# Optimization experiments

Measured on AMD Instinct MI355X. Metric: run time of the kernel, lower is better.

The kernel has to match this reference:

```python
import jax, jax.numpy as jnp
import numpy as np

TEMP = 0.07
POS_WINDOW = 2
EPS = 1e-8
NEG = -1e9  # finite large-negative for masking (safe under vjp)


def _l2norm(x):
    # matches F.normalize(dim=-1) with eps=1e-12
    n = jnp.sqrt(jnp.sum(x * x, axis=-1, keepdims=True))
    return x / jnp.maximum(n, 1e-12)


def setup_inputs() -> dict:
    key = jax.random.key(0)
    k1, k2, k3, k4, k5 = jax.random.split(key, 5)
    B, T, D = 32, 1024, 256
    eeg_enc = jax.random.normal(k1, (B, T, D), dtype=jnp.float32)
    eye_enc = jax.random.normal(k2, (B, T, D), dtype=jnp.float32)
    mask = jax.random.randint(k3, (B, T), 0, 2, dtype=jnp.int32)
    W_eeg = jax.random.normal(k4, (D, D), dtype=jnp.float32) / np.sqrt(D)
    W_eye = jax.random.normal(k5, (D, D), dtype=jnp.float32) / np.sqrt(D)
    return {"eeg_enc": eeg_enc, "eye_enc": eye_enc, "mask": mask,
            "W_eeg": W_eeg, "W_eye": W_eye}


def reference(eeg_enc, eye_enc, mask, W_eeg, W_eye):
    B, T, D = eeg_enc.shape
    valid = mask > 0  # (B,T)
    # nn.Linear(bias=False): x @ W.T, then L2-normalize
    e = _l2norm(jnp.einsum('btd,ed->bte', eeg_enc, W_eeg))
    v = _l2norm(jnp.einsum('btd,ed->bte', eye_enc, W_eye))
    sims = jnp.einsum('bid,bjd->bij', e, v) / TEMP  # (B,T,T)
    # rank of each valid step within the compressed (gathered) ordering
    rank = jnp.cumsum(valid.astype(jnp.int32), axis=-1) - 1  # (B,T)
    band = jnp.abs(rank[:, :, None] - rank[:, None, :]) <= POS_WINDOW
    pair = valid[:, :, None] & valid[:, None, :]  # both steps valid
    pos = pair & band
    # per-row max over positive (banded) entries
    pos_scores = jnp.max(jnp.where(pos, sims, NEG), axis=-1)  # (B,T)
    # logsumexp over valid columns (the gathered sims row)
    lse = jax.nn.logsumexp(jnp.where(valid[:, None, :], sims, NEG), axis=-1)
    row_loss = -(pos_scores - lse)  # (B,T)
    Tv = jnp.sum(valid, axis=-1)  # (B,)
    per_b = jnp.sum(jnp.where(valid, row_loss, 0.0), axis=-1) / jnp.maximum(Tv, 1)
    per_b = jnp.where(Tv >= 2, per_b, 0.0)  # skip samples with <2 valid steps
    return jnp.sum(per_b) / (B + EPS)
```

## Files before the change

### kernel.cpp

```cpp
#include <hip/hip_runtime.h>
#include <hip/hip_bf16.h>

typedef __attribute__((ext_vector_type(8))) short bf16x8;
typedef __attribute__((ext_vector_type(4))) float f32x4;

#define INVT (1.0f/0.07f)

static __device__ __forceinline__ short f2bf(float f){
    unsigned int u = __float_as_uint(f);
    unsigned int r = (u + 0x7fffu + ((u >> 16) & 1u)) >> 16;
    return (short)r;
}
static __device__ __forceinline__ float bf2f(short s){
    return __uint_as_float(((unsigned int)(unsigned short)s) << 16);
}

__global__ __launch_bounds__(256) void wconv_kernel(const float* __restrict__ Weeg,
                                                    const float* __restrict__ Weye,
                                                    short* __restrict__ Wout){
    int i = blockIdx.x * 256 + threadIdx.x;
    float v = (i < 65536) ? Weeg[i] : Weye[i - 65536];
    Wout[i] = f2bf(v);
}

__global__ __launch_bounds__(256) void rank_kernel(const int* __restrict__ mask,
                                                   int* __restrict__ rank,
                                                   int* __restrict__ idx,
                                                   int* __restrict__ Tv,
                                                   float* __restrict__ cb){
    __shared__ int ssum[256];
    int b = blockIdx.x, tid = threadIdx.x;
    int local[4]; int s = 0;
    #pragma unroll
    for (int q = 0; q < 4; ++q){
        int t = tid*4 + q;
        local[q] = (mask[b*1024 + t] > 0) ? 1 : 0;
        s += local[q];
    }
    ssum[tid] = s;
    __syncthreads();
    for (int off = 1; off < 256; off <<= 1){
        int add = (tid >= off) ? ssum[tid - off] : 0;
        __syncthreads();
        ssum[tid] += add;
        __syncthreads();
    }
    int run = ssum[tid] - s;
    #pragma unroll
    for (int q = 0; q < 4; ++q){
        int t = tid*4 + q;
        int g = b*1024 + t;
        run += local[q];
        rank[g] = run - 1;
        cb[g]   = local[q] ? 0.0f : -1e9f;
        if (local[q]) idx[b*1024 + run - 1] = t;
    }
    if (tid == 255) Tv[b] = ssum[255];
}

__global__ __launch_bounds__(256, 3) void proj_kernel(const float* __restrict__ Aeeg,
                                                      const float* __restrict__ Aeye,
                                                      const short* __restrict__ Wbf,
                                                      short* __restrict__ Eout,
                                                      short* __restrict__ Vout){
    __shared__ short sW[64 * 264];
    int sel = blockIdx.y;
    const float* A   = sel ? Aeye : Aeeg;
    const short* W   = Wbf + sel * 65536;
    short*       Out = sel ? Vout : Eout;

    int tid = threadIdx.x;
    int w = tid >> 6, lane = tid & 63;
    int l15 = lane & 15, lq = lane >> 4;
    int kb  = lq * 8;
    int row0 = blockIdx.x * 64;

    bf16x8 af[8];
    {
        const float* ap = A + (size_t)(row0 + w*16 + l15) * 256 + kb;
        #pragma unroll
        for (int g = 0; g < 8; ++g){
            float4 x0 = *(const float4*)(ap + g*32);
            float4 x1 = *(const float4*)(ap + g*32 + 4);
            bf16x8 t;
            t[0]=f2bf(x0.x); t[1]=f2bf(x0.y); t[2]=f2bf(x0.z); t[3]=f2bf(x0.w);
            t[4]=f2bf(x1.x); t[5]=f2bf(x1.y); t[6]=f2bf(x1.z); t[7]=f2bf(x1.w);
            af[g] = t;
        }
    }

    f32x4 acc[16];
    #pragma unroll
    for (int q = 0; q < 16; ++q) acc[q] = (f32x4){0.f,0.f,0.f,0.f};

    for (int pass = 0; pass < 4; ++pass){
        if (pass) __syncthreads();
        #pragma unroll
        for (int p = 0; p < 8; ++p){
            int flat = p*2048 + tid*8;
            int r = flat >> 8, c = flat & 255;
            *(int4*)&sW[r*264 + c] = *(const int4*)(W + (size_t)(pass*64 + r)*256 + c);
        }
        __syncthreads();
        #pragma unroll
        for (int nt = 0; nt < 4; ++nt){
            f32x4 c = acc[pass*4 + nt];
            const short* wp = &sW[(nt*16 + l15) * 264 + kb];
            #pragma unroll
            for (int g = 0; g < 8; ++g){
                bf16x8 bf = *(const bf16x8*)(wp + g*32);
                c = __builtin_amdgcn_mfma_f32_16x16x32_bf16(af[g], bf, c, 0, 0, 0);
            }
            acc[pass*4 + nt] = c;
        }
    }

    float scale[4];
    #pragma unroll
    for (int r = 0; r < 4; ++r){
        float ss = 0.f;
        #pragma unroll
        for (int q = 0; q < 16; ++q){ float x = acc[q][r]; ss += x*x; }
        ss += __shfl_xor(ss, 1);
        ss += __shfl_xor(ss, 2);
        ss += __shfl_xor(ss, 4);
        ss += __shfl_xor(ss, 8);
        scale[r] = 1.0f / fmaxf(sqrtf(ss), 1e-12f);
    }

    short* op = Out + (size_t)(row0 + w*16) * 256;
    #pragma unroll
    for (int q = 0; q < 16; ++q){
        #pragma unroll
        for (int r = 0; r < 4; ++r){
            op[(lq*4 + r) * 256 + q*16 + l15] = f2bf(acc[q][r] * scale[r]);
        }
    }
}

__global__ __launch_bounds__(256, 3) void loss_kernel(const short* __restrict__ E,
                                                      const short* __restrict__ V,
                                                      const float* __restrict__ cb,
                                                      float* __restrict__ psum){
    __shared__ short sV[64 * 264];
    __shared__ float sCb[256];

    int ib = blockIdx.x;
    int js = blockIdx.y;
    int b  = blockIdx.z;
    int i0 = ib * 128;

    int tid = threadIdx.x;
    int w = tid >> 6, lane = tid & 63;
    int l15 = lane & 15, lq = lane >> 4;
    int kb = lq * 8;

    sCb[tid] = cb[b*1024 + js*256 + tid];

    bf16x8 af0[8], af1[8];
    {
        const short* ep = E + ((size_t)b*1024 + i0 + w*32 + l15) * 256 + kb;
        #pragma unroll
        for (int g = 0; g < 8; ++g){
            af0[g] = *(const bf16x8*)(ep + g*32);
            af1[g] = *(const bf16x8*)(ep + 16*256 + g*32);
        }
    }

    float ls0[4] = {0.f,0.f,0.f,0.f};
    float ls1[4] = {0.f,0.f,0.f,0.f};
    const short* vb = V + ((size_t)b*1024 + js*256) * 256;

    for (int jc = 0; jc < 4; ++jc){
        __syncthreads();
        #pragma unroll
        for (int p = 0; p < 8; ++p){
            int flat = p*2048 + tid*8;
            int r = flat >> 8, c = flat & 255;
            *(int4*)&sV[r*264 + c] = *(const int4*)(vb + (size_t)(jc*64 + r)*256 + c);
        }
        __syncthreads();

        #pragma unroll
        for (int jt = 0; jt < 4; ++jt){
            f32x4 c0 = {0.f,0.f,0.f,0.f};
            f32x4 c1 = {0.f,0.f,0.f,0.f};
            const short* vp = &sV[(jt*16 + l15) * 264 + kb];
            #pragma unroll
            for (int g = 0; g < 8; ++g){
                bf16x8 bf = *(const bf16x8*)(vp + g*32);
                c0 = __builtin_amdgcn_mfma_f32_16x16x32_bf16(af0[g], bf, c0, 0, 0, 0);
                c1 = __builtin_amdgcn_mfma_f32_16x16x32_bf16(af1[g], bf, c1, 0, 0, 0);
            }
            float cbj = sCb[jc*64 + jt*16 + l15];
            #pragma unroll
            for (int r = 0; r < 4; ++r){
                ls0[r] += __expf(fmaf(c0[r], INVT, cbj));
                ls1[r] += __expf(fmaf(c1[r], INVT, cbj));
            }
        }
    }

    #pragma unroll
    for (int r = 0; r < 4; ++r){
        #pragma unroll
        for (int m = 1; m < 16; m <<= 1){
            ls0[r] += __shfl_xor(ls0[r], m);
            ls1[r] += __shfl_xor(ls1[r], m);
        }
    }
    if (l15 == 0){
        float* pp = psum + (((size_t)(b*4 + js)) << 10);
        int ibase = i0 + w*32 + lq*4;
        #pragma unroll
        for (int r = 0; r < 4; ++r){
            pp[ibase + r]      = ls0[r];
            pp[ibase + 16 + r] = ls1[r];
        }
    }
}

__global__ __launch_bounds__(256) void pos_kernel(const short* __restrict__ E,
                                                  const short* __restrict__ V,
                                                  const int* __restrict__ mask,
                                                  const int* __restrict__ rank,
                                                  const int* __restrict__ idx,
                                                  const int* __restrict__ Tv,
                                                  float* __restrict__ pmax){
    int tid = threadIdx.x;
    int gl  = tid & 15;
    int gid = (blockIdx.x * 256 + tid) >> 4;

    for (int q = 0; q < 8; ++q){
        int rf = gid + q * 4096;
        int b  = rf >> 10;
        if (mask[rf] > 0){
            int ri = rank[rf];
            int tv = Tv[b];
            int lo = ri - 2; if (lo < 0) lo = 0;
            int hi = ri + 2; if (hi > tv - 1) hi = tv - 1;

            const short* epp = E + (size_t)rf * 256 + gl * 16;
            float ev[16];
            {
                bf16x8 e0 = *(const bf16x8*)epp;
                bf16x8 e1 = *(const bf16x8*)(epp + 8);
                #pragma unroll
                for (int k = 0; k < 8; ++k){ ev[k] = bf2f(e0[k]); ev[8+k] = bf2f(e1[k]); }
            }
            float pm = -1e30f;
            for (int r = lo; r <= hi; ++r){
                int j = idx[b*1024 + r];
                const short* vpp = V + ((size_t)(b*1024) + j) * 256 + gl * 16;
                bf16x8 v0 = *(const bf16x8*)vpp;
                bf16x8 v1 = *(const bf16x8*)(vpp + 8);
                float s = 0.f;
                #pragma unroll
                for (int k = 0; k < 8; ++k){
                    s = fmaf(ev[k],   bf2f(v0[k]), s);
                    s = fmaf(ev[8+k], bf2f(v1[k]), s);
                }
                s += __shfl_xor(s, 1);
                s += __shfl_xor(s, 2);
                s += __shfl_xor(s, 4);
                s += __shfl_xor(s, 8);
                pm = fmaxf(pm, s);
            }
            if (gl == 0) pmax[rf] = pm * INVT;
        }
    }
}

__global__ __launch_bounds__(256) void reduce_kernel(const float* __restrict__ psum,
                                                     const float* __restrict__ pmax,
                                                     const int* __restrict__ mask,
                                                     const int* __restrict__ Tv,
                                                     float* __restrict__ per_b){
    __shared__ float sred[4];
    int b = blockIdx.x, tid = threadIdx.x;
    float a = 0.f;
    const float* pp = psum + (((size_t)(b*4)) << 10);
    #pragma unroll
    for (int q = 0; q < 4; ++q){
        int i = q*256 + tid;
        int g = b*1024 + i;
        if (mask[g] > 0){
            float ps = pp[i] + pp[i + 1024] + pp[i + 2048] + pp[i + 3072];
            a += logf(ps) - pmax[g];
        }
    }
    #pragma unroll
    for (int m = 1; m < 64; m <<= 1) a += __shfl_xor(a, m);
    if ((tid & 63) == 0) sred[tid >> 6] = a;
    __syncthreads();
    if (tid == 0){
        float t = sred[0] + sred[1] + sred[2] + sred[3];
        int tv = Tv[b];
        per_b[b] = (tv >= 2) ? t / (float)tv : 0.f;
    }
}

__global__ void final_kernel(const float* __restrict__ per_b,
                             float* __restrict__ out){
    int tid = threadIdx.x;
    float v = (tid < 32) ? per_b[tid] : 0.f;
    #pragma unroll
    for (int m = 1; m < 64; m <<= 1) v += __shfl_xor(v, m);
    if (tid == 0) out[0] = v / 32.0f;
}

extern "C" void kernel_launch(void* const* d_in, const int* in_sizes, int n_in,
                              void* d_out, int out_size, void* d_ws, size_t ws_size,
                              hipStream_t stream) {
    const float* eeg  = (const float*)d_in[0];
    const float* eye  = (const float*)d_in[1];
    const int*   mask = (const int*)d_in[2];
    const float* Weeg = (const float*)d_in[3];
    const float* Weye = (const float*)d_in[4];
    float* out = (float*)d_out;

    char* ws = (char*)d_ws;
    short* e_bf  = (short*)(ws);
    short* v_bf  = (short*)(ws + 16777216);
    short* wbf   = (short*)(ws + 33554432);
    int*   rank  = (int*)  (ws + 33816576);
    int*   idx   = (int*)  (ws + 33947648);
    float* cb    = (float*)(ws + 34078720);
    float* psum  = (float*)(ws + 34209792);
    float* pmax  = (float*)(ws + 34734080);
    int*   Tv    = (int*)  (ws + 34865152);
    float* per_b = (float*)(ws + 34865280);

    wconv_kernel<<<512, 256, 0, stream>>>(Weeg, Weye, wbf);
    rank_kernel<<<32, 256, 0, stream>>>(mask, rank, idx, Tv, cb);
    proj_kernel<<<dim3(512, 2), 256, 0, stream>>>(eeg, eye, wbf, e_bf, v_bf);
    loss_kernel<<<dim3(8, 4, 32), 256, 0, stream>>>(e_bf, v_bf, cb, psum);
    pos_kernel<<<256, 256, 0, stream>>>(e_bf, v_bf, mask, rank, idx, Tv, pmax);
    reduce_kernel<<<32, 256, 0, stream>>>(psum, pmax, mask, Tv, per_b);
    final_kernel<<<1, 64, 0, stream>>>(per_b, out);
}
```

Measured before the change: 186.6 us.

## Fuse prep kernels, transpose proj MFMA for vector stores, enlarge loss tile, flatten pos grid

Merges the weight-conversion and rank kernels into one launch to cut launch overhead. The projection now swaps the MFMA operands so each lane holds a row's outputs, which allows packed short4 stores and a two-step row-norm shuffle. The loss kernel processes 256 query rows per block instead of 128, reusing each shared V tile across four MFMA streams, with occupancy lowered to 2 blocks per SM to fit the extra registers. The positive-score kernel drops its inner loop and launches one 16-lane group per row across more blocks. The risk is register pressure in the loss kernel and fewer blocks in that grid.

```diff
diff --git a/kernel.cpp b/kernel.cpp
--- a/kernel.cpp
+++ b/kernel.cpp
@@ -15,21 +15,23 @@
     return __uint_as_float(((unsigned int)(unsigned short)s) << 16);
 }
 
-__global__ __launch_bounds__(256) void wconv_kernel(const float* __restrict__ Weeg,
-                                                    const float* __restrict__ Weye,
-                                                    short* __restrict__ Wout){
-    int i = blockIdx.x * 256 + threadIdx.x;
-    float v = (i < 65536) ? Weeg[i] : Weye[i - 65536];
-    Wout[i] = f2bf(v);
-}
-
-__global__ __launch_bounds__(256) void rank_kernel(const int* __restrict__ mask,
+__global__ __launch_bounds__(256) void prep_kernel(const float* __restrict__ Weeg,
+                                                   const float* __restrict__ Weye,
+                                                   const int* __restrict__ mask,
+                                                   short* __restrict__ Wout,
                                                    int* __restrict__ rank,
                                                    int* __restrict__ idx,
                                                    int* __restrict__ Tv,
                                                    float* __restrict__ cb){
     __shared__ int ssum[256];
-    int b = blockIdx.x, tid = threadIdx.x;
+    int tid = threadIdx.x;
+    if (blockIdx.x < 512){
+        int i = blockIdx.x * 256 + tid;
+        float v = (i < 65536) ? Weeg[i] : Weye[i - 65536];
+        Wout[i] = f2bf(v);
+        return;
+    }
+    int b = blockIdx.x - 512;
     int local[4]; int s = 0;
     #pragma unroll
     for (int q = 0; q < 4; ++q){
@@ -75,7 +77,7 @@
     int kb  = lq * 8;
     int row0 = blockIdx.x * 64;
 
-    bf16x8 af[8];
+    bf16x8 xf[8];
     {
         const float* ap = A + (size_t)(row0 + w*16 + l15) * 256 + kb;
         #pragma unroll
@@ -85,7 +87,7 @@
             bf16x8 t;
             t[0]=f2bf(x0.x); t[1]=f2bf(x0.y); t[2]=f2bf(x0.z); t[3]=f2bf(x0.w);
             t[4]=f2bf(x1.x); t[5]=f2bf(x1.y); t[6]=f2bf(x1.z); t[7]=f2bf(x1.w);
-            af[g] = t;
+            xf[g] = t;
         }
     }
 
@@ -93,6 +95,7 @@
     #pragma unroll
     for (int q = 0; q < 16; ++q) acc[q] = (f32x4){0.f,0.f,0.f,0.f};
 
+    #pragma unroll
     for (int pass = 0; pass < 4; ++pass){
         if (pass) __syncthreads();
         #pragma unroll
@@ -108,37 +111,36 @@
             const short* wp = &sW[(nt*16 + l15) * 264 + kb];
             #pragma unroll
             for (int g = 0; g < 8; ++g){
-                bf16x8 bf = *(const bf16x8*)(wp + g*32);
-                c = __builtin_amdgcn_mfma_f32_16x16x32_bf16(af[g], bf, c, 0, 0, 0);
+                bf16x8 wf = *(const bf16x8*)(wp + g*32);
+                c = __builtin_amdgcn_mfma_f32_16x16x32_bf16(wf, xf[g], c, 0, 0, 0);
             }
             acc[pass*4 + nt] = c;
         }
     }
 
-    float scale[4];
-    #pragma unroll
-    for (int r = 0; r < 4; ++r){
-        float ss = 0.f;
-        #pragma unroll
-        for (int q = 0; q < 16; ++q){ float x = acc[q][r]; ss += x*x; }
-        ss += __shfl_xor(ss, 1);
-        ss += __shfl_xor(ss, 2);
-        ss += __shfl_xor(ss, 4);
-        ss += __shfl_xor(ss, 8);
-        scale[r] = 1.0f / fmaxf(sqrtf(ss), 1e-12f);
-    }
-
-    short* op = Out + (size_t)(row0 + w*16) * 256;
+    float ss = 0.f;
     #pragma unroll
     for (int q = 0; q < 16; ++q){
         #pragma unroll
-        for (int r = 0; r < 4; ++r){
-            op[(lq*4 + r) * 256 + q*16 + l15] = f2bf(acc[q][r] * scale[r]);
-        }
-    }
-}
-
-__global__ __launch_bounds__(256, 3) void loss_kernel(const short* __restrict__ E,
+        for (int r = 0; r < 4; ++r){ float x = acc[q][r]; ss += x*x; }
+    }
+    ss += __shfl_xor(ss, 16);
+    ss += __shfl_xor(ss, 32);
+    float scale = 1.0f / fmaxf(sqrtf(ss), 1e-12f);
+
+    short* op = Out + (size_t)(row0 + w*16 + l15) * 256 + lq*4;
+    #pragma unroll
+    for (int q = 0; q < 16; ++q){
+        short4 pk;
+        pk.x = f2bf(acc[q][0] * scale);
+        pk.y = f2bf(acc[q][1] * scale);
+        pk.z = f2bf(acc[q][2] * scale);
+        pk.w = f2bf(acc[q][3] * scale);
+        *(short4*)(op + ((q >> 2) * 64 + (q & 3) * 16)) = pk;
+    }
+}
+
+__global__ __launch_bounds__(256, 2) void loss_kernel(const short* __restrict__ E,
                                                       const short* __restrict__ V,
                                                       const float* __restrict__ cb,
                                                       float* __restrict__ psum){
@@ -148,7 +150,7 @@
     int ib = blockIdx.x;
     int js = blockIdx.y;
     int b  = blockIdx.z;
-    int i0 = ib * 128;
+    int i0 = ib * 256;
 
     int tid = threadIdx.x;
     int w = tid >> 6, lane = tid & 63;
@@ -157,20 +159,26 @@
 
     sCb[tid] = cb[b*1024 + js*256 + tid];
 
-    bf16x8 af0[8], af1[8];
+    bf16x8 af[4][8];
     {
-        const short* ep = E + ((size_t)b*1024 + i0 + w*32 + l15) * 256 + kb;
-        #pragma unroll
-        for (int g = 0; g < 8; ++g){
-            af0[g] = *(const bf16x8*)(ep + g*32);
-            af1[g] = *(const bf16x8*)(ep + 16*256 + g*32);
-        }
-    }
-
-    float ls0[4] = {0.f,0.f,0.f,0.f};
-    float ls1[4] = {0.f,0.f,0.f,0.f};
+        const short* ep = E + ((size_t)b*1024 + i0 + w*64 + l15) * 256 + kb;
+        #pragma unroll
+        for (int s = 0; s < 4; ++s){
+            #pragma unroll
+            for (int g = 0; g < 8; ++g)
+                af[s][g] = *(const bf16x8*)(ep + s*16*256 + g*32);
+        }
+    }
+
+    float ls[4][4];
+    #pragma unroll
+    for (int s = 0; s < 4; ++s)
+        #pragma unroll
+        for (int r = 0; r < 4; ++r) ls[s][r] = 0.f;
+
     const short* vb = V + ((size_t)b*1024 + js*256) * 256;
 
+    #pragma unroll
     for (int jc = 0; jc < 4; ++jc){
         __syncthreads();
         #pragma unroll
@@ -185,37 +193,45 @@
         for (int jt = 0; jt < 4; ++jt){
             f32x4 c0 = {0.f,0.f,0.f,0.f};
             f32x4 c1 = {0.f,0.f,0.f,0.f};
+            f32x4 c2 = {0.f,0.f,0.f,0.f};
+            f32x4 c3 = {0.f,0.f,0.f,0.f};
             const short* vp = &sV[(jt*16 + l15) * 264 + kb];
             #pragma unroll
             for (int g = 0; g < 8; ++g){
                 bf16x8 bf = *(const bf16x8*)(vp + g*32);
-                c0 = __builtin_amdgcn_mfma_f32_16x16x32_bf16(af0[g], bf, c0, 0, 0, 0);
-                c1 = __builtin_amdgcn_mfma_f32_16x16x32_bf16(af1[g], bf, c1, 0, 0, 0);
+                c0 = __builtin_amdgcn_mfma_f32_16x16x32_bf16(af[0][g], bf, c0, 0, 0, 0);
+                c1 = __builtin_amdgcn_mfma_f32_16x16x32_bf16(af[1][g], bf, c1, 0, 0, 0);
+                c2 = __builtin_amdgcn_mfma_f32_16x16x32_bf16(af[2][g], bf, c2, 0, 0, 0);
+                c3 = __builtin_amdgcn_mfma_f32_16x16x32_bf16(af[3][g], bf, c3, 0, 0, 0);
             }
             float cbj = sCb[jc*64 + jt*16 + l15];
             #pragma unroll
             for (int r = 0; r < 4; ++r){
-                ls0[r] += __expf(fmaf(c0[r], INVT, cbj));
-                ls1[r] += __expf(fmaf(c1[r], INVT, cbj));
+                ls[0][r] += __expf(fmaf(c0[r], INVT, cbj));
+                ls[1][r] += __expf(fmaf(c1[r], INVT, cbj));
+                ls[2][r] += __expf(fmaf(c2[r], INVT, cbj));
+                ls[3][r] += __expf(fmaf(c3[r], INVT, cbj));
             }
         }
     }
 
     #pragma unroll
-    for (int r = 0; r < 4; ++r){
-        #pragma unroll
-        for (int m = 1; m < 16; m <<= 1){
-            ls0[r] += __shfl_xor(ls0[r], m);
-            ls1[r] += __shfl_xor(ls1[r], m);
+    for (int s = 0; s < 4; ++s){
+        #pragma unroll
+        for (int r = 0; r < 4; ++r){
+            #pragma unroll
+            for (int m = 1; m < 16; m <<= 1)
+                ls[s][r] += __shfl_xor(ls[s][r], m);
         }
     }
     if (l15 == 0){
         float* pp = psum + (((size_t)(b*4 + js)) << 10);
-        int ibase = i0 + w*32 + lq*4;
-        #pragma unroll
-        for (int r = 0; r < 4; ++r){
-            pp[ibase + r]      = ls0[r];
-            pp[ibase + 16 + r] = ls1[r];
+        int ibase = i0 + w*64 + lq*4;
+        #pragma unroll
+        for (int s = 0; s < 4; ++s){
+            #pragma unroll
+            for (int r = 0; r < 4; ++r)
+                pp[ibase + s*16 + r] = ls[s][r];
         }
     }
 }
@@ -229,46 +245,42 @@
                                                   float* __restrict__ pmax){
     int tid = threadIdx.x;
     int gl  = tid & 15;
-    int gid = (blockIdx.x * 256 + tid) >> 4;
-
-    for (int q = 0; q < 8; ++q){
-        int rf = gid + q * 4096;
-        int b  = rf >> 10;
-        if (mask[rf] > 0){
-            int ri = rank[rf];
-            int tv = Tv[b];
-            int lo = ri - 2; if (lo < 0) lo = 0;
-            int hi = ri + 2; if (hi > tv - 1) hi = tv - 1;
-
-            const short* epp = E + (size_t)rf * 256 + gl * 16;
-            float ev[16];
-            {
-                bf16x8 e0 = *(const bf16x8*)epp;
-                bf16x8 e1 = *(const bf16x8*)(epp + 8);
-                #pragma unroll
-                for (int k = 0; k < 8; ++k){ ev[k] = bf2f(e0[k]); ev[8+k] = bf2f(e1[k]); }
-            }
-            float pm = -1e30f;
-            for (int r = lo; r <= hi; ++r){
-                int j = idx[b*1024 + r];
-                const short* vpp = V + ((size_t)(b*1024) + j) * 256 + gl * 16;
-                bf16x8 v0 = *(const bf16x8*)vpp;
-                bf16x8 v1 = *(const bf16x8*)(vpp + 8);
-                float s = 0.f;
-                #pragma unroll
-                for (int k = 0; k < 8; ++k){
-                    s = fmaf(ev[k],   bf2f(v0[k]), s);
-                    s = fmaf(ev[8+k], bf2f(v1[k]), s);
-                }
-                s += __shfl_xor(s, 1);
-                s += __shfl_xor(s, 2);
-                s += __shfl_xor(s, 4);
-                s += __shfl_xor(s, 8);
-                pm = fmaxf(pm, s);
-            }
-            if (gl == 0) pmax[rf] = pm * INVT;
-        }
-    }
+    int rf  = (blockIdx.x * 256 + tid) >> 4;
+    int b   = rf >> 10;
+    if (mask[rf] <= 0) return;
+
+    int ri = rank[rf];
+    int tv = Tv[b];
+    int lo = ri - 2; if (lo < 0) lo = 0;
+    int hi = ri + 2; if (hi > tv - 1) hi = tv - 1;
+
+    const short* epp = E + (size_t)rf * 256 + gl * 16;
+    float ev[16];
+    {
+        bf16x8 e0 = *(const bf16x8*)epp;
+        bf16x8 e1 = *(const bf16x8*)(epp + 8);
+        #pragma unroll
+        for (int k = 0; k < 8; ++k){ ev[k] = bf2f(e0[k]); ev[8+k] = bf2f(e1[k]); }
+    }
+    float pm = -1e30f;
+    for (int r = lo; r <= hi; ++r){
+        int j = idx[b*1024 + r];
+        const short* vpp = V + ((size_t)(b*1024) + j) * 256 + gl * 16;
+        bf16x8 v0 = *(const bf16x8*)vpp;
+        bf16x8 v1 = *(const bf16x8*)(vpp + 8);
+        float s = 0.f;
+        #pragma unroll
+        for (int k = 0; k < 8; ++k){
+            s = fmaf(ev[k],   bf2f(v0[k]), s);
+            s = fmaf(ev[8+k], bf2f(v1[k]), s);
+        }
+        s += __shfl_xor(s, 1);
+        s += __shfl_xor(s, 2);
+        s += __shfl_xor(s, 4);
+        s += __shfl_xor(s, 8);
+        pm = fmaxf(pm, s);
+    }
+    if (gl == 0) pmax[rf] = pm * INVT;
 }
 
 __global__ __launch_bounds__(256) void reduce_kernel(const float* __restrict__ psum,
@@ -331,11 +343,10 @@
     int*   Tv    = (int*)  (ws + 34865152);
     float* per_b = (float*)(ws + 34865280);
 
-    wconv_kernel<<<512, 256, 0, stream>>>(Weeg, Weye, wbf);
-    rank_kernel<<<32, 256, 0, stream>>>(mask, rank, idx, Tv, cb);
+    prep_kernel<<<544, 256, 0, stream>>>(Weeg, Weye, mask, wbf, rank, idx, Tv, cb);
     proj_kernel<<<dim3(512, 2), 256, 0, stream>>>(eeg, eye, wbf, e_bf, v_bf);
-    loss_kernel<<<dim3(8, 4, 32), 256, 0, stream>>>(e_bf, v_bf, cb, psum);
-    pos_kernel<<<256, 256, 0, stream>>>(e_bf, v_bf, mask, rank, idx, Tv, pmax);
+    loss_kernel<<<dim3(4, 4, 32), 256, 0, stream>>>(e_bf, v_bf, cb, psum);
+    pos_kernel<<<2048, 256, 0, stream>>>(e_bf, v_bf, mask, rank, idx, Tv, pmax);
     reduce_kernel<<<32, 256, 0, stream>>>(psum, pmax, mask, Tv, per_b);
     final_kernel<<<1, 64, 0, stream>>>(per_b, out);
 }
```

New measurement: 177.5 us. 1.05x faster.
